# Kernel optimization log

Measured on AMD Instinct MI355X. Metric: run time of the kernel, lower is better.

Reference implementation:

```python
import jax, jax.numpy as jnp
import numpy as np

SEM_DIM = 256
AC_DIM = 36
CODEBOOK_SIZE = 8192
FSQ_LEVELS = 21
COMMIT_COST = 0.25
HALF = (FSQ_LEVELS - 1) / 2.0  # 10.0
EPS = 0.001


def setup_inputs() -> dict:
    key = jax.random.key(0)
    k1, k2 = jax.random.split(key)
    z = jax.random.normal(k1, (8, SEM_DIM + AC_DIM, 4096), dtype=jnp.float32)
    lim = 1.0 / CODEBOOK_SIZE
    codebook = jax.random.uniform(k2, (CODEBOOK_SIZE, SEM_DIM), dtype=jnp.float32,
                                  minval=-lim, maxval=lim)
    return {"z": z, "codebook": codebook}


def _round_ste(x):
    return x + jax.lax.stop_gradient(jnp.round(x) - x)


def _vq(z_sem, codebook):
    # z_sem: (B, D, T), codebook: (K, D)
    B, D, T = z_sem.shape
    z_flat = jnp.transpose(z_sem, (0, 2, 1)).reshape(B * T, D)  # (N, D)
    # pairwise squared distances via matmul: ||z||^2 - 2 z.W^T + ||W||^2
    dists = (jnp.sum(z_flat * z_flat, axis=1, keepdims=True)
             - 2.0 * jnp.matmul(z_flat, codebook.T)
             + jnp.sum(codebook * codebook, axis=1)[None, :])  # (N, K)
    indices = jnp.argmin(dists, axis=1)  # (N,)
    z_q_flat = codebook[indices]  # (N, D) gather
    z_q = jnp.transpose(z_q_flat.reshape(B, T, D), (0, 2, 1))  # (B, D, T)
    codebook_loss = jnp.mean((z_q - jax.lax.stop_gradient(z_sem)) ** 2)
    commitment_loss = COMMIT_COST * jnp.mean((jax.lax.stop_gradient(z_q) - z_sem) ** 2)
    loss = codebook_loss + commitment_loss
    z_q_ste = z_sem + jax.lax.stop_gradient(z_q - z_sem)  # straight-through
    return z_q_ste, indices.reshape(B, T), loss


def _fsq(z_ac):
    z_b = jnp.tanh(z_ac) * (HALF + EPS)
    z_q = _round_ste(z_b)
    codes = jnp.clip((z_q + HALF).astype(jnp.int32), 0, FSQ_LEVELS - 1)
    return z_q, codes


def reference(z, codebook):
    z_sem = z[:, :SEM_DIM, :]
    z_ac = z[:, SEM_DIM:, :]
    z_sem_q, sem_indices, vq_loss = _vq(z_sem, codebook)
    z_ac_q, ac_codes = _fsq(z_ac)
    z_q = jnp.concatenate([z_sem_q, z_ac_q], axis=1)
    return (z_q, sem_indices, ac_codes, vq_loss, z_ac_q)
```

## Files before the change

kernel.cpp:

```cpp
#include <hip/hip_runtime.h>
#include <math.h>

#define BB 8
#define DSEM 256
#define DAC 36
#define DTOT 292
#define TT 4096
#define NCB 8192
#define NROWS (BB*TT)

static constexpr size_t O0 = 0;
static constexpr size_t O1 = 9568256;
static constexpr size_t O2 = 9601024;
static constexpr size_t O3 = 10780672;
static constexpr size_t O4 = 10780673;

static constexpr size_t WB_AH   = 0;
static constexpr size_t WB_BH   = 16777216;
static constexpr size_t WB_TMIN = 20971520;
static constexpr size_t WB_CBT  = 37748736;
static constexpr size_t WB_RN   = 46137344;
static constexpr size_t WB_CSQ  = 46268416;
static constexpr size_t WB_LOSS = 46301184;
static constexpr size_t WB_CNT  = 46301192;
static constexpr size_t WB_END  = 46301200;
static constexpr unsigned WL_CAP = 4194304;

typedef _Float16 f16x8 __attribute__((ext_vector_type(8)));
typedef __attribute__((ext_vector_type(4))) float f32x4;

__device__ __forceinline__ void gload_lds16(const void* g, void* lds) {
  __builtin_amdgcn_global_load_lds(
      (const __attribute__((address_space(1))) void*)g,
      (__attribute__((address_space(3))) void*)lds, 16, 0, 0);
}


__global__ __launch_bounds__(256) void k_csq(const float* __restrict__ cb,
                                             float* __restrict__ csq,
                                             double* __restrict__ loss,
                                             unsigned* __restrict__ counter) {
  if (blockIdx.x == 0 && threadIdx.x == 0) { loss[0] = 0.0; counter[0] = 0u; }
  int w = (blockIdx.x << 2) + (threadIdx.x >> 6);
  int lane = threadIdx.x & 63;
  float4 v = *reinterpret_cast<const float4*>(cb + (size_t)w * DSEM + lane * 4);
  float s = v.x * v.x + v.y * v.y + v.z * v.z + v.w * v.w;
  for (int off = 32; off; off >>= 1) s += __shfl_xor(s, off);
  if (lane == 0) csq[w] = s;
}

__global__ __launch_bounds__(256) void k_rn(const float* __restrict__ z,
                                            float* __restrict__ rn) {
  int r = blockIdx.x * 256 + threadIdx.x;
  int b = r >> 12, t = r & 4095;
  const float* p = z + ((size_t)(b * DTOT) << 12) + t;
  double acc = 0.0;
  #pragma unroll 8
  for (int d = 0; d < DSEM; ++d) {
    float v = p[(size_t)d << 12];
    acc += (double)v * (double)v;
  }
  rn[r] = (float)acc;
}

__global__ __launch_bounds__(256) void k_fsq(const float* __restrict__ z,
                                             float* __restrict__ out) {
  int e = blockIdx.x * 256 + threadIdx.x;
  int b = e / (DAC * TT);
  int rem = e - b * (DAC * TT);
  int d = rem >> 12, t = rem & 4095;
  float zv = z[((size_t)(b * DTOT + DSEM + d) << 12) + t];
  float th = (float)tanh((double)zv);
  float zb = th * 10.001f;
  float zq = rintf(zb);
  int code = (int)(zq + 10.0f);
  code = code < 0 ? 0 : (code > 20 ? 20 : code);
  out[O0 + (((size_t)(b * DTOT + DSEM + d)) << 12) + t] = zq;
  out[O2 + e] = (float)code;
  out[O4 + e] = zq;
}

__global__ void k_fin(const double* __restrict__ loss, float* __restrict__ out3) {
  out3[0] = (float)(1.25 * loss[0] / 8388608.0);
}


__global__ __launch_bounds__(256) void k_prepA(const float* __restrict__ z,
                                               _Float16* __restrict__ Ah,
                                               float* __restrict__ outz) {
  __shared__ float tile[64][65];
  int bid = blockIdx.x;
  int tt = bid & 63, kt = (bid >> 6) & 3, b = bid >> 8;
  int k0 = kt * 64, t0 = tt * 64;
  int tid = threadIdx.x;
  #pragma unroll
  for (int i = 0; i < 16; ++i) {
    int flat = i * 256 + tid;
    int kk = flat >> 6, t2 = flat & 63;
    tile[kk][t2] = z[((size_t)(b * DTOT + k0 + kk) << 12) + t0 + t2];
  }
  __syncthreads();
  float* zTb = outz + (size_t)b * (DTOT * TT);
  #pragma unroll
  for (int i = 0; i < 16; ++i) {
    int flat = i * 256 + tid;
    int t2 = flat >> 6, kk = flat & 63;
    float v = tile[kk][t2];
    Ah[(size_t)(b * 4096 + t0 + t2) * 256 + k0 + kk] = (_Float16)v;
    zTb[(size_t)(t0 + t2) * 256 + k0 + kk] = v;
  }
}

__global__ __launch_bounds__(256) void k_prepB(const float* __restrict__ cb,
                                               _Float16* __restrict__ Bh) {
  int e = blockIdx.x * 256 + threadIdx.x;
  Bh[e] = (_Float16)(cb[e] * -32768.0f);
}

__global__ __launch_bounds__(256) void k_prepC(const float* __restrict__ cb,
                                               float* __restrict__ cbT4) {
  int e = blockIdx.x * 256 + threadIdx.x;
  int c = e & 31, r = e >> 5;
  int u = r >> 6, k4 = r & 63;
  int j = (u << 5) + c;
  float4 v = *reinterpret_cast<const float4*>(cb + (size_t)j * 256 + k4 * 4);
  reinterpret_cast<float4*>(cbT4)[e] = v;
}

__global__ __launch_bounds__(256) void k_gemm(const _Float16* __restrict__ A,
                                              const _Float16* __restrict__ B,
                                              const float* __restrict__ csq,
                                              _Float16* __restrict__ tmin) {
  __shared__ char smraw[128 * 68 * 4];
  _Float16* As = (_Float16*)smraw;
  _Float16* Bs = (_Float16*)(smraw + 16384);
  float* red = (float*)smraw;
  const float SCALE = 6.103515625e-05f;

  int bid = blockIdx.x;
  int wg = (bid & 7) * 2048 + (bid >> 3);
  int mtile = wg >> 6, ntile = wg & 63;
  int rbase = mtile << 7, cbase = ntile << 7;
  int tid = threadIdx.x, lane = tid & 63, wid = tid >> 6;
  int wm = wid >> 1, wn = wid & 1;
  int l15 = lane & 15, l4 = lane >> 4;

  f32x4 acc[4][4];
  #pragma unroll
  for (int mi = 0; mi < 4; ++mi)
    #pragma unroll
    for (int ni = 0; ni < 4; ++ni) acc[mi][ni] = (f32x4){0.f, 0.f, 0.f, 0.f};

  for (int kt = 0; kt < 4; ++kt) {
    int kb = kt << 6;
    __syncthreads();
    #pragma unroll
    for (int i = 0; i < 4; ++i) {
      int flat = (wid * 4 + i) * 64 + lane;
      int row = flat >> 3, kk = (flat & 7) << 3;
      gload_lds16(A + (size_t)(rbase + row) * 256 + kb + kk, (char*)As + flat * 16);
      gload_lds16(B + (size_t)(cbase + row) * 256 + kb + kk, (char*)Bs + flat * 16);
    }
    __syncthreads();
    #pragma unroll
    for (int ks = 0; ks < 2; ++ks) {
      int ko = (ks << 5) + (l4 << 3);
      f16x8 af[4], bv[4];
      #pragma unroll
      for (int mi = 0; mi < 4; ++mi)
        af[mi] = *(const f16x8*)(As + ((wm * 64 + mi * 16 + l15) << 6) + ko);
      #pragma unroll
      for (int ni = 0; ni < 4; ++ni)
        bv[ni] = *(const f16x8*)(Bs + ((wn * 64 + ni * 16 + l15) << 6) + ko);
      #pragma unroll
      for (int mi = 0; mi < 4; ++mi)
        #pragma unroll
        for (int ni = 0; ni < 4; ++ni)
          acc[mi][ni] = __builtin_amdgcn_mfma_f32_16x16x32_f16(af[mi], bv[ni], acc[mi][ni], 0, 0, 0);
    }
  }

  float csv[4];
  #pragma unroll
  for (int ni = 0; ni < 4; ++ni) csv[ni] = csq[cbase + wn * 64 + ni * 16 + l15];

  __syncthreads();
  #pragma unroll
  for (int mi = 0; mi < 4; ++mi) {
    #pragma unroll
    for (int r = 0; r < 4; ++r) {
      int row = wm * 64 + mi * 16 + l4 * 4 + r;
      float v0 = fminf(fmaf(acc[mi][0][r], SCALE, csv[0]),
                       fmaf(acc[mi][1][r], SCALE, csv[1]));
      float v1 = fminf(fmaf(acc[mi][2][r], SCALE, csv[2]),
                       fmaf(acc[mi][3][r], SCALE, csv[3]));
      red[row * 68 + (wn * 2 + 0) * 16 + l15] = v0;
      red[row * 68 + (wn * 2 + 1) * 16 + l15] = v1;
    }
  }
  __syncthreads();
  if (tid < 128) {
    int row = tid;
    const float* rp = red + row * 68;
    union { _Float16 h[4]; short4 s; } uu;
    #pragma unroll
    for (int q = 0; q < 4; ++q) {
      float m = rp[q * 16];
      #pragma unroll
      for (int x = 1; x < 16; ++x) m = fminf(m, rp[q * 16 + x]);
      uu.h[q] = (_Float16)m;
    }
    *reinterpret_cast<short4*>(tmin + (size_t)(rbase + row) * 256 + ntile * 4) = uu.s;
  }
}

__global__ __launch_bounds__(256) void k_cand(const _Float16* __restrict__ tmin,
                                              unsigned* __restrict__ wl,
                                              unsigned* __restrict__ counter,
                                              unsigned long long* __restrict__ result) {
  __shared__ unsigned long long smask[16][4];
  __shared__ unsigned scnt[16];
  __shared__ unsigned soff[16];
  int tid = threadIdx.x;
  int wv = tid >> 6, lane = tid & 63;
  int row0 = blockIdx.x << 4;

  for (int rr = wv; rr < 16; rr += 4) {
    int row = row0 + rr;
    const _Float16* tp = tmin + (size_t)row * 256;
    float v[4];
    #pragma unroll
    for (int i = 0; i < 4; ++i) v[i] = (float)tp[i * 64 + lane];
    float g = fminf(fminf(v[0], v[1]), fminf(v[2], v[3]));
    #pragma unroll
    for (int off = 32; off; off >>= 1) g = fminf(g, __shfl_xor(g, off));
    float thr = g + 2e-4f;
    if (lane == 0) result[row] = 0xFFFFFFFFFFFFFFFFULL;
    unsigned cnt = 0;
    #pragma unroll
    for (int i = 0; i < 4; ++i) {
      unsigned long long mask = __ballot(v[i] <= thr);
      if (lane == 0) smask[rr][i] = mask;
      cnt += (unsigned)__popcll(mask);
    }
    if (lane == 0) scnt[rr] = cnt;
  }
  __syncthreads();
  if (tid == 0) {
    unsigned tot = 0;
    #pragma unroll
    for (int r = 0; r < 16; ++r) { soff[r] = tot; tot += scnt[r]; }
    unsigned base = atomicAdd(counter, tot);
    #pragma unroll
    for (int r = 0; r < 16; ++r) soff[r] += base;
  }
  __syncthreads();
  for (int rr = wv; rr < 16; rr += 4) {
    int row = row0 + rr;
    unsigned off = soff[rr];
    unsigned acc = 0;
    #pragma unroll
    for (int i = 0; i < 4; ++i) {
      unsigned long long mask = smask[rr][i];
      bool c = (mask >> lane) & 1ULL;
      if (c) {
        unsigned rank = acc + (unsigned)__popcll(mask & ((1ULL << lane) - 1ULL));
        unsigned idx = off + rank;
        if (idx < WL_CAP) wl[idx] = ((unsigned)row << 8) | (unsigned)(i * 64 + lane);
      }
      acc += (unsigned)__popcll(mask);
    }
  }
}

__global__ __launch_bounds__(256) void k_scan(const float* __restrict__ zT,
                                              const float* __restrict__ cbT4,
                                              const float* __restrict__ csq,
                                              const float* __restrict__ rn,
                                              const unsigned* __restrict__ wl,
                                              const unsigned* __restrict__ counter,
                                              unsigned long long* __restrict__ result) {
  unsigned total = *counter;
  if (total > WL_CAP) total = WL_CAP;
  int tid = threadIdx.x;
  int gw = blockIdx.x * 4 + (tid >> 6);
  int half = (tid >> 5) & 1, l32 = tid & 31;
  for (unsigned it = (unsigned)(gw * 2 + half); it < total; it += 16384u) {
    unsigned e = wl[it];
    int row = (int)(e >> 8), u = (int)(e & 255u);
    int j = (u << 5) + l32;
    int b = row >> 12, t = row & 4095;
    const float4* zp = reinterpret_cast<const float4*>(
        zT + (size_t)b * (DTOT * TT) + (size_t)t * 256);
    const float4* cp = reinterpret_cast<const float4*>(cbT4) + ((u * 64) * 32 + l32);
    float an = rn[row], cq = csq[j];
    float m0 = 0.f, m1 = 0.f, m2 = 0.f, m3 = 0.f;
    #pragma unroll 8
    for (int k4 = 0; k4 < 64; ++k4) {
      float4 cv = cp[k4 * 32];
      float4 zv = zp[k4];
      m0 = fmaf(zv.x, cv.x, m0);
      m1 = fmaf(zv.y, cv.y, m1);
      m2 = fmaf(zv.z, cv.z, m2);
      m3 = fmaf(zv.w, cv.w, m3);
    }
    float m = (m0 + m1) + (m2 + m3);
    float d = (an - 2.f * m) + cq;
    unsigned long long pk =
        (((unsigned long long)__float_as_uint(d)) << 32) | (unsigned)j;
    #pragma unroll
    for (int off = 16; off; off >>= 1) {
      unsigned long long o = __shfl_xor(pk, off);
      if (o < pk) pk = o;
    }
    if (l32 == 0) atomicMin(result + row, pk);
  }
}

__global__ __launch_bounds__(256) void k_loss(const float* __restrict__ z,
                                              const float* __restrict__ cb,
                                              const unsigned long long* __restrict__ result,
                                              float* __restrict__ out0,
                                              float* __restrict__ out1,
                                              double* __restrict__ loss) {
  int e0 = blockIdx.x * 256 + threadIdx.x;
  if (e0 < NROWS) out1[e0] = (float)(unsigned)(result[e0] & 0xFFFFFFFFULL);
  float s = 0.f;
  for (int e = e0; e < BB * DSEM * TT; e += 2048 * 256) {
    int b = e >> 20;
    int rem = e & 1048575;
    int d = rem >> 12, t = rem & 4095;
    int r = (b << 12) + t;
    int j = (int)(unsigned)(result[r] & 0xFFFFFFFFULL);
    float c = cb[(size_t)j * DSEM + d];
    size_t zi = ((size_t)(b * DTOT + d) << 12) + t;
    float zv = z[zi];
    out0[zi] = c;
    float df = c - zv;
    s += df * df;
  }
  for (int off = 32; off; off >>= 1) s += __shfl_xor(s, off);
  __shared__ float ws4[4];
  int lane = threadIdx.x & 63, w = threadIdx.x >> 6;
  if (lane == 0) ws4[w] = s;
  __syncthreads();
  if (threadIdx.x == 0) {
    float tot = ws4[0] + ws4[1] + ws4[2] + ws4[3];
    atomicAdd(loss, (double)tot);
  }
}


__global__ __launch_bounds__(256) void k_vq(const float* __restrict__ z,
                                            const float* __restrict__ cb,
                                            const float* __restrict__ csq,
                                            const float* __restrict__ rn,
                                            float* __restrict__ pmin,
                                            int* __restrict__ pidx) {
  __shared__ float As[32][132];
  __shared__ float Bs[32][132];
  const int tid = threadIdx.x;
  const int tx = tid & 15, ty = tid >> 4;
  const int mb = blockIdx.x >> 2, s = blockIdx.x & 3;
  const int r0 = mb << 7;
  const int b = r0 >> 12, t0 = r0 & 4095;
  const int nbase = s * 2048;

  int mrow[8], jcol[8];
  #pragma unroll
  for (int i = 0; i < 4; ++i) {
    mrow[i] = ty * 4 + i;  mrow[i + 4] = 64 + ty * 4 + i;
    jcol[i] = tx * 4 + i;  jcol[i + 4] = 64 + tx * 4 + i;
  }
  float an[8];
  #pragma unroll
  for (int i = 0; i < 8; ++i) an[i] = rn[r0 + mrow[i]];

  float rmin[8]; int ridx[8];
  #pragma unroll
  for (int i = 0; i < 8; ++i) { rmin[i] = 3.402823466e38f; ridx[i] = 0; }

  for (int nc = 0; nc < 16; ++nc) {
    const int n0 = nbase + nc * 128;
    float acc[8][8];
    #pragma unroll
    for (int i = 0; i < 8; ++i)
      #pragma unroll
      for (int j = 0; j < 8; ++j) acc[i][j] = 0.f;

    for (int kc = 0; kc < 8; ++kc) {
      const int kb = kc << 5;
      __syncthreads();
      #pragma unroll
      for (int i = 0; i < 4; ++i) {
        int flat = i * 256 + tid;
        int k = flat >> 5, m4 = (flat & 31) << 2;
        float4 vv = *reinterpret_cast<const float4*>(
            z + ((size_t)(b * DTOT + kb + k) << 12) + t0 + m4);
        *reinterpret_cast<float4*>(&As[k][m4]) = vv;
      }
      #pragma unroll
      for (int i = 0; i < 4; ++i) {
        int flat = i * 256 + tid;
        int j = flat >> 3, k4 = (flat & 7) << 2;
        float4 vv = *reinterpret_cast<const float4*>(
            cb + ((size_t)(n0 + j) << 8) + kb + k4);
        Bs[k4 + 0][j] = vv.x; Bs[k4 + 1][j] = vv.y;
        Bs[k4 + 2][j] = vv.z; Bs[k4 + 3][j] = vv.w;
      }
      __syncthreads();
      #pragma unroll 8
      for (int k = 0; k < 32; ++k) {
        float a[8], bv[8];
        *reinterpret_cast<float4*>(&a[0]) = *reinterpret_cast<const float4*>(&As[k][ty * 4]);
        *reinterpret_cast<float4*>(&a[4]) = *reinterpret_cast<const float4*>(&As[k][64 + ty * 4]);
        *reinterpret_cast<float4*>(&bv[0]) = *reinterpret_cast<const float4*>(&Bs[k][tx * 4]);
        *reinterpret_cast<float4*>(&bv[4]) = *reinterpret_cast<const float4*>(&Bs[k][64 + tx * 4]);
        #pragma unroll
        for (int i = 0; i < 8; ++i)
          #pragma unroll
          for (int j = 0; j < 8; ++j) acc[i][j] = fmaf(a[i], bv[j], acc[i][j]);
      }
    }
    float cs[8];
    #pragma unroll
    for (int j = 0; j < 8; ++j) cs[j] = csq[n0 + jcol[j]];
    #pragma unroll
    for (int i = 0; i < 8; ++i) {
      #pragma unroll
      for (int j = 0; j < 8; ++j) {
        float d = (an[i] - 2.f * acc[i][j]) + cs[j];
        int jg = n0 + jcol[j];
        if (d < rmin[i] || (d == rmin[i] && jg < ridx[i])) { rmin[i] = d; ridx[i] = jg; }
      }
    }
  }
  __syncthreads();
  float* redf = &As[0][0];
  int* redi = reinterpret_cast<int*>(&Bs[0][0]);
  #pragma unroll
  for (int i = 0; i < 8; ++i) {
    redf[mrow[i] * 16 + tx] = rmin[i];
    redi[mrow[i] * 16 + tx] = ridx[i];
  }
  __syncthreads();
  if (tid < 128) {
    int row = tid;
    float bestv = redf[row * 16]; int bi = redi[row * 16];
    #pragma unroll
    for (int x = 1; x < 16; ++x) {
      float m = redf[row * 16 + x]; int ii = redi[row * 16 + x];
      if (m < bestv || (m == bestv && ii < bi)) { bestv = m; bi = ii; }
    }
    pmin[(size_t)(r0 + row) * 4 + s] = bestv;
    pidx[(size_t)(r0 + row) * 4 + s] = bi;
  }
}

__global__ __launch_bounds__(256) void k_comb(const float* __restrict__ pmin,
                                              const int* __restrict__ pidx,
                                              int* __restrict__ widx,
                                              float* __restrict__ out1) {
  int r = blockIdx.x * 256 + threadIdx.x;
  float best = pmin[r * 4]; int bi = pidx[r * 4];
  #pragma unroll
  for (int s2 = 1; s2 < 4; ++s2) {
    float m = pmin[r * 4 + s2]; int ii = pidx[r * 4 + s2];
    if (m < best || (m == best && ii < bi)) { best = m; bi = ii; }
  }
  widx[r] = bi;
  out1[r] = (float)bi;
}

__global__ __launch_bounds__(256) void k_loss_fb(const float* __restrict__ z,
                                                 const float* __restrict__ cb,
                                                 const int* __restrict__ idx,
                                                 float* __restrict__ out0,
                                                 double* __restrict__ loss) {
  float s = 0.f;
  for (int e = blockIdx.x * 256 + threadIdx.x; e < BB * DSEM * TT; e += 2048 * 256) {
    int b = e >> 20;
    int rem = e & 1048575;
    int d = rem >> 12, t = rem & 4095;
    int r = (b << 12) + t;
    int j = idx[r];
    float c = cb[(size_t)j * DSEM + d];
    size_t zi = ((size_t)(b * DTOT + d) << 12) + t;
    float zv = z[zi];
    out0[zi] = c;
    float df = c - zv;
    s += df * df;
  }
  for (int off = 32; off; off >>= 1) s += __shfl_xor(s, off);
  __shared__ float ws4[4];
  int lane = threadIdx.x & 63, w = threadIdx.x >> 6;
  if (lane == 0) ws4[w] = s;
  __syncthreads();
  if (threadIdx.x == 0) {
    float tot = ws4[0] + ws4[1] + ws4[2] + ws4[3];
    atomicAdd(loss, (double)tot);
  }
}


extern "C" void kernel_launch(void* const* d_in, const int* in_sizes, int n_in,
                              void* d_out, int out_size, void* d_ws, size_t ws_size,
                              hipStream_t stream) {
  const float* z  = (const float*)d_in[0];
  const float* cb = (const float*)d_in[1];
  float* out = (float*)d_out;

  if (ws_size >= WB_END) {
    char* wsb = (char*)d_ws;
    _Float16* Ah   = (_Float16*)(wsb + WB_AH);
    _Float16* Bh   = (_Float16*)(wsb + WB_BH);
    _Float16* tmin = (_Float16*)(wsb + WB_TMIN);
    float*    cbT4 = (float*)(wsb + WB_CBT);
    float*    rn   = (float*)(wsb + WB_RN);
    float*    csq  = (float*)(wsb + WB_CSQ);
    double*   loss = (double*)(wsb + WB_LOSS);
    unsigned* counter = (unsigned*)(wsb + WB_CNT);
    unsigned* wl = (unsigned*)(wsb + WB_AH);
    unsigned long long* result = (unsigned long long*)(wsb + WB_BH);
    float* zT = out + O0;

    k_csq<<<NCB / 4, 256, 0, stream>>>(cb, csq, loss, counter);
    k_rn<<<NROWS / 256, 256, 0, stream>>>(z, rn);
    k_fsq<<<(BB * DAC * TT) / 256, 256, 0, stream>>>(z, out);
    k_prepA<<<2048, 256, 0, stream>>>(z, Ah, zT);
    k_prepB<<<8192, 256, 0, stream>>>(cb, Bh);
    k_prepC<<<2048, 256, 0, stream>>>(cb, cbT4);
    k_gemm<<<16384, 256, 0, stream>>>(Ah, Bh, csq, tmin);
    k_cand<<<NROWS / 16, 256, 0, stream>>>(tmin, wl, counter, result);
    k_scan<<<2048, 256, 0, stream>>>(zT, cbT4, csq, rn, wl, counter, result);
    k_loss<<<2048, 256, 0, stream>>>(z, cb, result, out + O0, out + O1, loss);
    k_fin<<<1, 1, 0, stream>>>(loss, out + O3);
  } else {
    float* wsf = (float*)d_ws;
    float* csq  = wsf;
    float* rn   = wsf + 8192;
    float* pmin = wsf + 40960;
    int*   pidx = (int*)(wsf + 172032);
    int*   widx = (int*)(wsf + 303104);
    double* loss = (double*)(wsf + 335872);
    unsigned* counter = (unsigned*)(wsf + 335876);

    k_csq<<<NCB / 4, 256, 0, stream>>>(cb, csq, loss, counter);
    k_rn<<<NROWS / 256, 256, 0, stream>>>(z, rn);
    k_fsq<<<(BB * DAC * TT) / 256, 256, 0, stream>>>(z, out);
    k_vq<<<(NROWS / 128) * 4, 256, 0, stream>>>(z, cb, csq, rn, pmin, pidx);
    k_comb<<<NROWS / 256, 256, 0, stream>>>(pmin, pidx, widx, out + O1);
    k_loss_fb<<<2048, 256, 0, stream>>>(z, cb, widx, out + O0, loss);
    k_fin<<<1, 1, 0, stream>>>(loss, out + O3);
  }
}
```

Baseline: 411.9 us.

## Fuse codebook prep kernels, swizzle GEMM LDS layout, fold final loss into k_loss

Measured after the change: 442.5 us. +7.4%, slower.

```diff
diff --git a/kernel.cpp b/kernel.cpp
--- a/kernel.cpp
+++ b/kernel.cpp
@@ -35,19 +35,6 @@
       (__attribute__((address_space(3))) void*)lds, 16, 0, 0);
 }
 
-
-__global__ __launch_bounds__(256) void k_csq(const float* __restrict__ cb,
-                                             float* __restrict__ csq,
-                                             double* __restrict__ loss,
-                                             unsigned* __restrict__ counter) {
-  if (blockIdx.x == 0 && threadIdx.x == 0) { loss[0] = 0.0; counter[0] = 0u; }
-  int w = (blockIdx.x << 2) + (threadIdx.x >> 6);
-  int lane = threadIdx.x & 63;
-  float4 v = *reinterpret_cast<const float4*>(cb + (size_t)w * DSEM + lane * 4);
-  float s = v.x * v.x + v.y * v.y + v.z * v.z + v.w * v.w;
-  for (int off = 32; off; off >>= 1) s += __shfl_xor(s, off);
-  if (lane == 0) csq[w] = s;
-}
 
 __global__ __launch_bounds__(256) void k_rn(const float* __restrict__ z,
                                             float* __restrict__ rn) {
@@ -80,10 +67,27 @@
   out[O4 + e] = zq;
 }
 
-__global__ void k_fin(const double* __restrict__ loss, float* __restrict__ out3) {
-  out3[0] = (float)(1.25 * loss[0] / 8388608.0);
-}
-
+
+__global__ __launch_bounds__(256) void k_prepB2(const float* __restrict__ cb,
+                                                _Float16* __restrict__ Bh,
+                                                float* __restrict__ csq,
+                                                double* __restrict__ loss,
+                                                unsigned* __restrict__ counters) {
+  if (blockIdx.x == 0 && threadIdx.x == 0) {
+    loss[0] = 0.0; counters[0] = 0u; counters[1] = 0u;
+  }
+  int e = blockIdx.x * 256 + threadIdx.x;
+  float4 v = reinterpret_cast<const float4*>(cb)[e];
+  union { _Float16 h[4]; short4 s4; } o;
+  o.h[0] = (_Float16)(v.x * -32768.0f);
+  o.h[1] = (_Float16)(v.y * -32768.0f);
+  o.h[2] = (_Float16)(v.z * -32768.0f);
+  o.h[3] = (_Float16)(v.w * -32768.0f);
+  reinterpret_cast<short4*>(Bh)[e] = o.s4;
+  float s = v.x * v.x + v.y * v.y + v.z * v.z + v.w * v.w;
+  for (int off = 32; off; off >>= 1) s += __shfl_xor(s, off);
+  if ((threadIdx.x & 63) == 0) csq[e >> 6] = s;
+}
 
 __global__ __launch_bounds__(256) void k_prepA(const float* __restrict__ z,
                                                _Float16* __restrict__ Ah,
@@ -109,12 +113,6 @@
     Ah[(size_t)(b * 4096 + t0 + t2) * 256 + k0 + kk] = (_Float16)v;
     zTb[(size_t)(t0 + t2) * 256 + k0 + kk] = v;
   }
-}
-
-__global__ __launch_bounds__(256) void k_prepB(const float* __restrict__ cb,
-                                               _Float16* __restrict__ Bh) {
-  int e = blockIdx.x * 256 + threadIdx.x;
-  Bh[e] = (_Float16)(cb[e] * -32768.0f);
 }
 
 __global__ __launch_bounds__(256) void k_prepC(const float* __restrict__ cb,
@@ -144,6 +142,7 @@
   int tid = threadIdx.x, lane = tid & 63, wid = tid >> 6;
   int wm = wid >> 1, wn = wid & 1;
   int l15 = lane & 15, l4 = lane >> 4;
+  int sw = l15 & 7;
 
   f32x4 acc[4][4];
   #pragma unroll
@@ -157,21 +156,24 @@
     #pragma unroll
     for (int i = 0; i < 4; ++i) {
       int flat = (wid * 4 + i) * 64 + lane;
-      int row = flat >> 3, kk = (flat & 7) << 3;
-      gload_lds16(A + (size_t)(rbase + row) * 256 + kb + kk, (char*)As + flat * 16);
-      gload_lds16(B + (size_t)(cbase + row) * 256 + kb + kk, (char*)Bs + flat * 16);
+      int row = flat >> 3;
+      int csrc = (flat & 7) ^ (row & 7);
+      gload_lds16(A + (size_t)(rbase + row) * 256 + kb + (csrc << 3),
+                  (char*)As + flat * 16);
+      gload_lds16(B + (size_t)(cbase + row) * 256 + kb + (csrc << 3),
+                  (char*)Bs + flat * 16);
     }
     __syncthreads();
     #pragma unroll
     for (int ks = 0; ks < 2; ++ks) {
-      int ko = (ks << 5) + (l4 << 3);
+      int off = ((((ks << 2) + l4) ^ sw) << 3);
       f16x8 af[4], bv[4];
       #pragma unroll
       for (int mi = 0; mi < 4; ++mi)
-        af[mi] = *(const f16x8*)(As + ((wm * 64 + mi * 16 + l15) << 6) + ko);
+        af[mi] = *(const f16x8*)(As + ((wm * 64 + mi * 16 + l15) << 6) + off);
       #pragma unroll
       for (int ni = 0; ni < 4; ++ni)
-        bv[ni] = *(const f16x8*)(Bs + ((wn * 64 + ni * 16 + l15) << 6) + ko);
+        bv[ni] = *(const f16x8*)(Bs + ((wn * 64 + ni * 16 + l15) << 6) + off);
       #pragma unroll
       for (int mi = 0; mi < 4; ++mi)
         #pragma unroll
@@ -322,7 +324,9 @@
                                               const unsigned long long* __restrict__ result,
                                               float* __restrict__ out0,
                                               float* __restrict__ out1,
-                                              double* __restrict__ loss) {
+                                              double* __restrict__ loss,
+                                              unsigned* __restrict__ done,
+                                              float* __restrict__ out3) {
   int e0 = blockIdx.x * 256 + threadIdx.x;
   if (e0 < NROWS) out1[e0] = (float)(unsigned)(result[e0] & 0xFFFFFFFFULL);
   float s = 0.f;
@@ -347,9 +351,32 @@
   if (threadIdx.x == 0) {
     float tot = ws4[0] + ws4[1] + ws4[2] + ws4[3];
     atomicAdd(loss, (double)tot);
-  }
-}
-
+    __threadfence();
+    unsigned old = atomicAdd(done, 1u);
+    if (old == 2047u) {
+      double total = atomicAdd(loss, 0.0);
+      out3[0] = (float)(1.25 * total / 8388608.0);
+    }
+  }
+}
+
+
+__global__ __launch_bounds__(256) void k_csq(const float* __restrict__ cb,
+                                             float* __restrict__ csq,
+                                             double* __restrict__ loss,
+                                             unsigned* __restrict__ counter) {
+  if (blockIdx.x == 0 && threadIdx.x == 0) { loss[0] = 0.0; counter[0] = 0u; }
+  int w = (blockIdx.x << 2) + (threadIdx.x >> 6);
+  int lane = threadIdx.x & 63;
+  float4 v = *reinterpret_cast<const float4*>(cb + (size_t)w * DSEM + lane * 4);
+  float s = v.x * v.x + v.y * v.y + v.z * v.z + v.w * v.w;
+  for (int off = 32; off; off >>= 1) s += __shfl_xor(s, off);
+  if (lane == 0) csq[w] = s;
+}
+
+__global__ void k_fin(const double* __restrict__ loss, float* __restrict__ out3) {
+  out3[0] = (float)(1.25 * loss[0] / 8388608.0);
+}
 
 __global__ __launch_bounds__(256) void k_vq(const float* __restrict__ z,
                                             const float* __restrict__ cb,
@@ -519,22 +546,21 @@
     float*    rn   = (float*)(wsb + WB_RN);
     float*    csq  = (float*)(wsb + WB_CSQ);
     double*   loss = (double*)(wsb + WB_LOSS);
-    unsigned* counter = (unsigned*)(wsb + WB_CNT);
+    unsigned* counters = (unsigned*)(wsb + WB_CNT);
     unsigned* wl = (unsigned*)(wsb + WB_AH);
     unsigned long long* result = (unsigned long long*)(wsb + WB_BH);
     float* zT = out + O0;
 
-    k_csq<<<NCB / 4, 256, 0, stream>>>(cb, csq, loss, counter);
+    k_prepB2<<<2048, 256, 0, stream>>>(cb, Bh, csq, loss, counters);
     k_rn<<<NROWS / 256, 256, 0, stream>>>(z, rn);
     k_fsq<<<(BB * DAC * TT) / 256, 256, 0, stream>>>(z, out);
     k_prepA<<<2048, 256, 0, stream>>>(z, Ah, zT);
-    k_prepB<<<8192, 256, 0, stream>>>(cb, Bh);
     k_prepC<<<2048, 256, 0, stream>>>(cb, cbT4);
     k_gemm<<<16384, 256, 0, stream>>>(Ah, Bh, csq, tmin);
-    k_cand<<<NROWS / 16, 256, 0, stream>>>(tmin, wl, counter, result);
-    k_scan<<<2048, 256, 0, stream>>>(zT, cbT4, csq, rn, wl, counter, result);
-    k_loss<<<2048, 256, 0, stream>>>(z, cb, result, out + O0, out + O1, loss);
-    k_fin<<<1, 1, 0, stream>>>(loss, out + O3);
+    k_cand<<<NROWS / 16, 256, 0, stream>>>(tmin, wl, counters, result);
+    k_scan<<<2048, 256, 0, stream>>>(zT, cbT4, csq, rn, wl, counters, result);
+    k_loss<<<2048, 256, 0, stream>>>(z, cb, result, out + O0, out + O1, loss,
+                                     counters + 1, out + O3);
   } else {
     float* wsf = (float*)d_ws;
     float* csq  = wsf;
```
